# Performance work log

Hardware: AMD Instinct MI355X
Metric: run time of the kernel (lower is better)

## Reference

```python
import math
import jax, jax.numpy as jnp
import numpy as np

CHUNK = 32
PROB_FLOOR = 0.02
EPS = 1e-5

def l2norm(x):
    return x * jax.lax.rsqrt(jnp.sum(x * x, -1, keepdims=True) + 1e-6)

def causal_dwconv(x, w):
    # x: (B, L, C), w: (C, K) depthwise causal FIR (left-padded)
    B, L, C = x.shape
    K = w.shape[-1]
    y = jax.lax.conv_general_dilated(jnp.transpose(x, (0, 2, 1)), w[:, None, :], (1,), [(K - 1, 0)], feature_group_count=C)
    return jnp.transpose(y, (0, 2, 1))

def delta_rule_chunkwise(q, k, v, beta, chunk=CHUNK):
    # q,k: (b,h,L,dk)  v: (b,h,L,dv)  beta: (b,h,L)
    b, h, L, dk = q.shape
    dv = v.shape[-1]
    pad = (-L) % chunk
    if pad:
        q = jnp.pad(q, ((0, 0), (0, 0), (0, pad), (0, 0)))
        k = jnp.pad(k, ((0, 0), (0, 0), (0, pad), (0, 0)))
        v = jnp.pad(v, ((0, 0), (0, 0), (0, pad), (0, 0)))
        beta = jnp.pad(beta, ((0, 0), (0, 0), (0, pad)))
    Lp = L + pad
    n = Lp // chunk
    q = l2norm(q)
    k = l2norm(k)
    v = v * beta[..., None]
    kb = k * beta[..., None]
    r = lambda t: t.reshape(b, h, n, chunk, t.shape[-1])
    q, k, v, kb = (r(q), r(k), r(v), r(kb))
    i_ = jnp.arange(chunk)
    strict_lower = (i_[:, None] > i_[None, :]).astype(q.dtype)
    lower_incl = (i_[:, None] >= i_[None, :]).astype(q.dtype)
    inv = -(kb @ jnp.swapaxes(k, -1, -2)) * strict_lower  # (b,h,n,c,c)
    for i in range(1, chunk):  # row-wise forward substitution; chunk is static so unrolled
        inv = inv.at[..., i, :].add(jnp.einsum('...j,...jk->...k', inv[..., i, :], inv))
    inv = inv + jnp.eye(chunk, dtype=q.dtype)
    u = inv @ v   # (b,h,n,c,dv)
    w = inv @ kb  # (b,h,n,c,dk)
    mv = lambda t: jnp.moveaxis(t, 2, 0)  # scan over chunks
    def step(S, xs):
        qi, ki, ui, wi = xs
        attn = (qi @ jnp.swapaxes(ki, -1, -2)) * lower_incl
        ui2 = ui - wi @ S
        oi = qi @ S + attn @ ui2
        return S + jnp.swapaxes(ki, -1, -2) @ ui2, oi
    S0 = jnp.zeros((b, h, dk, dv), q.dtype)
    S, outs = jax.lax.scan(step, S0, (mv(q), mv(k), mv(u), mv(w)))
    out = jnp.moveaxis(outs, 0, 2).reshape(b, h, Lp, dv)[:, :, :L]
    return out, S

def head_stats(x):
    # x: (B,L,H,D) -> (B,L,4): [mean, var, abs-mean, l2] per head, averaged over heads
    mean = x.mean(-1)
    var = ((x - mean[..., None]) ** 2).mean(-1)
    am = jnp.abs(x).mean(-1)
    l2 = jnp.sqrt((x * x).sum(-1))
    return jnp.stack([mean, var, am, l2], -1).mean(2)

def rmsnorm(x, w):
    return x * jax.lax.rsqrt((x * x).mean(-1, keepdims=True) + EPS) * w

def setup_inputs():
    key = jax.random.key(0)
    ks = jax.random.split(key, 20)
    B, L, D, H = 2, 4096, 1024, 4
    dv = D // H
    f32 = jnp.float32
    rn = lambda k, shape, s: (jax.random.normal(k, shape) * s).astype(f32)
    fir = lambda k, shape: rn(k, shape, 0.02).at[..., -1].add(1.0)  # near-identity causal filter
    return {
        'hidden_states': jax.random.normal(ks[0], (B, L, D), f32),
        'Wq': rn(ks[1], (D, D), 0.02), 'Wk': rn(ks[2], (D, D), 0.02), 'Wv': rn(ks[3], (D, D), 0.02),
        'Wb': rn(ks[4], (D, H), 0.02),
        'wq_conv': fir(ks[5], (D, 4)), 'wk_conv': fir(ks[6], (D, 4)), 'wv_conv': fir(ks[7], (D, 4)),
        'fir_long': fir(ks[8], (H, dv, 64)), 'fir_short': fir(ks[9], (H, dv, 5)),
        'Wg1': rn(ks[10], (D + 16, D), 0.02), 'bg1': jnp.zeros((D,), f32),
        'Wg2': rn(ks[11], (D, 4), 0.02), 'bg2': jnp.array([-0.5, -0.5, 1.0, 3.0], f32),
        'logit_temp': jnp.array([math.log(math.expm1(0.7))], f32),
        'conv_res_logit': jnp.full((H,), -1.0, f32),
        'Wres': rn(ks[12], (D, H), 0.02), 'bres': jnp.full((H,), -1.0, f32),
        'Wog1': rn(ks[13], (D + 8, D // 2), 0.02), 'bog1': jnp.zeros((D // 2,), f32),
        'Wog2': rn(ks[14], (D // 2, 1), 0.02), 'bog2': jnp.full((1,), -1.0986122886681098, f32),
        'norm_w': jnp.ones((dv,), f32),
        'Wo': rn(ks[15], (D, D), 0.02),
    }

def reference(hidden_states, Wq, Wk, Wv, Wb, wq_conv, wk_conv, wv_conv, fir_long, fir_short, Wg1, bg1, Wg2, bg2, logit_temp, conv_res_logit, Wres, bres, Wog1, bog1, Wog2, bog2, norm_w, Wo):
    B, L, D = hidden_states.shape
    H = Wb.shape[-1]
    silu = jax.nn.silu
    q_in = silu(causal_dwconv(hidden_states @ Wq, wq_conv))
    k_in = silu(causal_dwconv(hidden_states @ Wk, wk_conv))
    v_in = silu(causal_dwconv(hidden_states @ Wv, wv_conv))
    dk = q_in.shape[-1] // H
    dv = v_in.shape[-1] // H
    q = q_in.reshape(B, L, H, dk)
    k = k_in.reshape(B, L, H, dk)
    v_direct = v_in.reshape(B, L, H, dv)
    beta = jax.nn.sigmoid(hidden_states @ Wb)  # (B,L,H)
    do, S = delta_rule_chunkwise(jnp.transpose(q, (0, 2, 1, 3)), jnp.transpose(k, (0, 2, 1, 3)), jnp.transpose(v_direct, (0, 2, 1, 3)), jnp.transpose(beta, (0, 2, 1)))
    delta_out = jnp.transpose(do, (0, 2, 1, 3))  # (B,L,H,dv)
    local_long = causal_dwconv(v_in, fir_long.reshape(-1, fir_long.shape[-1])).reshape(B, L, H, dv)
    local_short = causal_dwconv(v_in, fir_short.reshape(-1, fir_short.shape[-1])).reshape(B, L, H, dv)
    stats = jnp.concatenate([head_stats(t) for t in (local_short, local_long, delta_out, v_direct)], -1)  # (B,L,16)
    gate_in = jnp.concatenate([hidden_states, stats], -1)
    logits = (jax.nn.gelu(gate_in @ Wg1 + bg1, approximate=False) @ Wg2 + bg2) / jax.nn.softplus(logit_temp)
    p = jax.nn.softmax(logits, -1)
    p = jnp.clip(p, PROB_FLOOR, None)
    p = p / p.sum(-1, keepdims=True)
    pw = p[:, :, None, :]  # (B,L,1,4)
    o = pw[..., 0:1] * local_short + pw[..., 1:2] * local_long + pw[..., 2:3] * delta_out + pw[..., 3:4] * v_direct
    res_gate = jax.nn.sigmoid(hidden_states @ Wres + bres)  # (B,L,H)
    static = jax.nn.sigmoid(conv_res_logit)  # (H,)
    o = o + (static[None, None, :] * res_gate)[..., None] * local_short
    og_stats = jnp.concatenate([head_stats(o), head_stats(v_direct)], -1)  # (B,L,8)
    og_in = jnp.concatenate([hidden_states, og_stats], -1)
    og = jax.nn.sigmoid(jax.nn.gelu(og_in @ Wog1 + bog1, approximate=False) @ Wog2 + bog2)  # (B,L,1)
    o = o * og[:, :, :, None]
    o = rmsnorm(o, norm_w)
    return o.reshape(B, L, -1) @ Wo
```

## Files before the change

### kernel.cpp

```cpp
#include <hip/hip_runtime.h>
#include <math.h>

#define B_ 2
#define L_ 4096
#define D_ 1024
#define H_ 4
#define DH 256
#define CHUNKSZ 32
#define NCH (L_/CHUNKSZ)
#define BL (B_*L_)
#define BLD (B_*L_*D_)

typedef __attribute__((ext_vector_type(8))) short bf16x8;
typedef __attribute__((ext_vector_type(4))) float f32x4;

__device__ __forceinline__ float sigmf(float x) { return 1.f / (1.f + expf(-x)); }
__device__ __forceinline__ float geluf(float x) { return 0.5f * x * (1.f + erff(x * 0.70710678118654752f)); }
__device__ __forceinline__ unsigned short f2bf(float f) {
  unsigned int u = __float_as_uint(f);
  unsigned int r = (u + 0x7FFFu + ((u >> 16) & 1u)) >> 16;
  return (unsigned short)r;
}
__device__ __forceinline__ unsigned int pk2bf(float a, float b) {
  return ((unsigned int)f2bf(b) << 16) | (unsigned int)f2bf(a);
}

__global__ __launch_bounds__(256)
void wconv_all(const float* __restrict__ Wq, const float* __restrict__ Wk,
               const float* __restrict__ Wv, const float* __restrict__ Wg1,
               const float* __restrict__ Wog1, const float* __restrict__ Wo,
               unsigned short* __restrict__ wtq, unsigned short* __restrict__ wtk,
               unsigned short* __restrict__ wtv, unsigned short* __restrict__ wtg1,
               unsigned short* __restrict__ wtog1, unsigned short* __restrict__ wto) {
  __shared__ float tile[32][33];
  int bid = blockIdx.x;
  const float* W; unsigned short* Wt; int N; int rem;
  if (bid < 5120) {
    int widx = bid >> 10; rem = bid & 1023; N = 1024;
    switch (widx) {
      case 0: W = Wq; Wt = wtq; break;
      case 1: W = Wk; Wt = wtk; break;
      case 2: W = Wv; Wt = wtv; break;
      case 3: W = Wg1; Wt = wtg1; break;
      default: W = Wo; Wt = wto; break;
    }
  } else { rem = bid - 5120; N = 512; W = Wog1; Wt = wtog1; }
  int nT = N >> 5;
  int nb = (rem % nT) * 32, kb = (rem / nT) * 32;
  int tx = threadIdx.x & 31, ty = threadIdx.x >> 5;
  for (int i = 0; i < 32; i += 8)
    tile[ty + i][tx] = W[(long)(kb + ty + i) * N + nb + tx];
  __syncthreads();
  for (int i = 0; i < 32; i += 8)
    Wt[(long)(nb + ty + i) * 1024 + kb + tx] = f2bf(tile[tx][ty + i]);
}

__global__ __launch_bounds__(256)
void cvt_beta(const float* __restrict__ hs, unsigned short* __restrict__ hsb,
              const float* __restrict__ Wb, const float* __restrict__ Wres,
              const float* __restrict__ bres,
              float* __restrict__ beta, float* __restrict__ resg) {
  __shared__ float red[4][8];
  long m = blockIdx.x;
  int tid = threadIdx.x;
  int k0 = tid * 4;
  float4 x = *reinterpret_cast<const float4*>(&hs[m * 1024 + k0]);
  ushort4 o;
  o.x = f2bf(x.x); o.y = f2bf(x.y); o.z = f2bf(x.z); o.w = f2bf(x.w);
  *reinterpret_cast<ushort4*>(&hsb[m * 1024 + k0]) = o;
  float xr[4] = {x.x, x.y, x.z, x.w};
  float ab[4] = {0.f, 0.f, 0.f, 0.f}, ar[4] = {0.f, 0.f, 0.f, 0.f};
#pragma unroll
  for (int j = 0; j < 4; ++j) {
    float4 wb = *reinterpret_cast<const float4*>(&Wb[(long)(k0 + j) * 4]);
    float4 wr = *reinterpret_cast<const float4*>(&Wres[(long)(k0 + j) * 4]);
    ab[0] = fmaf(xr[j], wb.x, ab[0]); ab[1] = fmaf(xr[j], wb.y, ab[1]);
    ab[2] = fmaf(xr[j], wb.z, ab[2]); ab[3] = fmaf(xr[j], wb.w, ab[3]);
    ar[0] = fmaf(xr[j], wr.x, ar[0]); ar[1] = fmaf(xr[j], wr.y, ar[1]);
    ar[2] = fmaf(xr[j], wr.z, ar[2]); ar[3] = fmaf(xr[j], wr.w, ar[3]);
  }
#pragma unroll
  for (int st = 32; st > 0; st >>= 1) {
#pragma unroll
    for (int n = 0; n < 4; ++n) { ab[n] += __shfl_xor(ab[n], st); ar[n] += __shfl_xor(ar[n], st); }
  }
  int w = tid >> 6;
  if ((tid & 63) == 0) {
#pragma unroll
    for (int n = 0; n < 4; ++n) { red[w][n] = ab[n]; red[w][n + 4] = ar[n]; }
  }
  __syncthreads();
  if (tid < 8) {
    float s = red[0][tid] + red[1][tid] + red[2][tid] + red[3][tid];
    if (tid < 4) beta[m * 4 + tid] = sigmf(s);
    else resg[m * 4 + tid - 4] = sigmf(s + bres[tid - 4]);
  }
}

__global__ __launch_bounds__(256)
void gemm_qkv(const unsigned short* __restrict__ A, const unsigned short* __restrict__ Bt,
              float* __restrict__ C0) {
  __shared__ unsigned short Al[128 * 32];
  __shared__ unsigned short Bl[128 * 32];
  const int K = 1024;
  const int nBn = 24;
  int wgid = blockIdx.x;
  int xcd = wgid & 7;
  int local = wgid >> 3;
  int bm = (xcd * 8 + local / nBn) * 128;
  int bn = (local % nBn) * 128;
  float* Cd = C0 + (long)(bn >> 10) * BLD;
  int cbn = bn & 1023;
  int tid = threadIdx.x;
  int lane = tid & 63, wid = tid >> 6;
  int wr = wid >> 1, wc = wid & 1;
  int l15 = lane & 15, l4 = lane >> 4;
  f32x4 acc[4][4];
#pragma unroll
  for (int i = 0; i < 4; ++i)
#pragma unroll
    for (int j = 0; j < 4; ++j) { acc[i][j].x = 0.f; acc[i][j].y = 0.f; acc[i][j].z = 0.f; acc[i][j].w = 0.f; }
  for (int k0 = 0; k0 < K; k0 += 32) {
    __syncthreads();
#pragma unroll
    for (int i = 0; i < 2; ++i) {
      int idx = tid + i * 256;
      int r = idx >> 2, sl = idx & 3;
      int src = sl ^ ((r >> 1) & 3);
      __builtin_amdgcn_global_load_lds(
          (const __attribute__((address_space(1))) unsigned int*)&A[(long)(bm + r) * K + k0 + src * 8],
          (__attribute__((address_space(3))) unsigned int*)&Al[idx * 8], 16, 0, 0);
      __builtin_amdgcn_global_load_lds(
          (const __attribute__((address_space(1))) unsigned int*)&Bt[(long)(bn + r) * K + k0 + src * 8],
          (__attribute__((address_space(3))) unsigned int*)&Bl[idx * 8], 16, 0, 0);
    }
    __syncthreads();
    bf16x8 af[4], bfr[4];
#pragma unroll
    for (int fi = 0; fi < 4; ++fi) {
      int r = wr * 64 + fi * 16 + l15;
      af[fi] = *reinterpret_cast<const bf16x8*>(&Al[r * 32 + (l4 ^ ((r >> 1) & 3)) * 8]);
    }
#pragma unroll
    for (int fj = 0; fj < 4; ++fj) {
      int r = wc * 64 + fj * 16 + l15;
      bfr[fj] = *reinterpret_cast<const bf16x8*>(&Bl[r * 32 + (l4 ^ ((r >> 1) & 3)) * 8]);
    }
#pragma unroll
    for (int fi = 0; fi < 4; ++fi)
#pragma unroll
      for (int fj = 0; fj < 4; ++fj)
        acc[fi][fj] = __builtin_amdgcn_mfma_f32_16x16x32_bf16(af[fi], bfr[fj], acc[fi][fj], 0, 0, 0);
  }
#pragma unroll
  for (int fi = 0; fi < 4; ++fi) {
    int rb = bm + wr * 64 + fi * 16 + l4 * 4;
#pragma unroll
    for (int fj = 0; fj < 4; ++fj) {
      int cb = cbn + wc * 64 + fj * 16 + l15;
#pragma unroll
      for (int j = 0; j < 4; ++j)
        Cd[(long)(rb + j) * 1024 + cb] = acc[fi][fj][j];
    }
  }
}

__global__ __launch_bounds__(256)
void gemm_gateog(const unsigned short* __restrict__ A, const unsigned short* __restrict__ Bt,
                 float* __restrict__ Cg, float* __restrict__ Cog) {
  __shared__ unsigned short Al[128 * 32];
  __shared__ unsigned short Bl[128 * 32];
  const int K = 1024;
  const int nBn = 12;
  int wgid = blockIdx.x;
  int xcd = wgid & 7;
  int local = wgid >> 3;
  int bm = (xcd * 8 + local / nBn) * 128;
  int bn = (local % nBn) * 128;
  float* Cd; int stride, cbn;
  if (bn < 1024) { Cd = Cg; stride = 1024; cbn = bn; }
  else { Cd = Cog; stride = 512; cbn = bn - 1024; }
  int tid = threadIdx.x;
  int lane = tid & 63, wid = tid >> 6;
  int wr = wid >> 1, wc = wid & 1;
  int l15 = lane & 15, l4 = lane >> 4;
  f32x4 acc[4][4];
#pragma unroll
  for (int i = 0; i < 4; ++i)
#pragma unroll
    for (int j = 0; j < 4; ++j) { acc[i][j].x = 0.f; acc[i][j].y = 0.f; acc[i][j].z = 0.f; acc[i][j].w = 0.f; }
  for (int k0 = 0; k0 < K; k0 += 32) {
    __syncthreads();
#pragma unroll
    for (int i = 0; i < 2; ++i) {
      int idx = tid + i * 256;
      int r = idx >> 2, sl = idx & 3;
      int src = sl ^ ((r >> 1) & 3);
      __builtin_amdgcn_global_load_lds(
          (const __attribute__((address_space(1))) unsigned int*)&A[(long)(bm + r) * K + k0 + src * 8],
          (__attribute__((address_space(3))) unsigned int*)&Al[idx * 8], 16, 0, 0);
      __builtin_amdgcn_global_load_lds(
          (const __attribute__((address_space(1))) unsigned int*)&Bt[(long)(bn + r) * K + k0 + src * 8],
          (__attribute__((address_space(3))) unsigned int*)&Bl[idx * 8], 16, 0, 0);
    }
    __syncthreads();
    bf16x8 af[4], bfr[4];
#pragma unroll
    for (int fi = 0; fi < 4; ++fi) {
      int r = wr * 64 + fi * 16 + l15;
      af[fi] = *reinterpret_cast<const bf16x8*>(&Al[r * 32 + (l4 ^ ((r >> 1) & 3)) * 8]);
    }
#pragma unroll
    for (int fj = 0; fj < 4; ++fj) {
      int r = wc * 64 + fj * 16 + l15;
      bfr[fj] = *reinterpret_cast<const bf16x8*>(&Bl[r * 32 + (l4 ^ ((r >> 1) & 3)) * 8]);
    }
#pragma unroll
    for (int fi = 0; fi < 4; ++fi)
#pragma unroll
      for (int fj = 0; fj < 4; ++fj)
        acc[fi][fj] = __builtin_amdgcn_mfma_f32_16x16x32_bf16(af[fi], bfr[fj], acc[fi][fj], 0, 0, 0);
  }
#pragma unroll
  for (int fi = 0; fi < 4; ++fi) {
    int rb = bm + wr * 64 + fi * 16 + l4 * 4;
#pragma unroll
    for (int fj = 0; fj < 4; ++fj) {
      int cb = cbn + wc * 64 + fj * 16 + l15;
#pragma unroll
      for (int j = 0; j < 4; ++j)
        Cd[(long)(rb + j) * stride + cb] = acc[fi][fj][j];
    }
  }
}

__global__ __launch_bounds__(256)
void gemm_bf16(const unsigned short* __restrict__ A, const unsigned short* __restrict__ Bt,
               float* __restrict__ C, int N) {
  __shared__ unsigned short Al[128 * 32];
  __shared__ unsigned short Bl[128 * 32];
  const int K = 1024;
  int nBn = N >> 7;
  int wgid = blockIdx.x;
  int xcd = wgid & 7;
  int local = wgid >> 3;
  int bm = (xcd * 8 + local / nBn) * 128;
  int bn = (local % nBn) * 128;
  int tid = threadIdx.x;
  int lane = tid & 63, wid = tid >> 6;
  int wr = wid >> 1, wc = wid & 1;
  int l15 = lane & 15, l4 = lane >> 4;
  f32x4 acc[4][4];
#pragma unroll
  for (int i = 0; i < 4; ++i)
#pragma unroll
    for (int j = 0; j < 4; ++j) { acc[i][j].x = 0.f; acc[i][j].y = 0.f; acc[i][j].z = 0.f; acc[i][j].w = 0.f; }
  for (int k0 = 0; k0 < K; k0 += 32) {
    __syncthreads();
#pragma unroll
    for (int i = 0; i < 2; ++i) {
      int idx = tid + i * 256;
      int r = idx >> 2, sl = idx & 3;
      int src = sl ^ ((r >> 1) & 3);
      __builtin_amdgcn_global_load_lds(
          (const __attribute__((address_space(1))) unsigned int*)&A[(long)(bm + r) * K + k0 + src * 8],
          (__attribute__((address_space(3))) unsigned int*)&Al[idx * 8], 16, 0, 0);
      __builtin_amdgcn_global_load_lds(
          (const __attribute__((address_space(1))) unsigned int*)&Bt[(long)(bn + r) * K + k0 + src * 8],
          (__attribute__((address_space(3))) unsigned int*)&Bl[idx * 8], 16, 0, 0);
    }
    __syncthreads();
    bf16x8 af[4], bfr[4];
#pragma unroll
    for (int fi = 0; fi < 4; ++fi) {
      int r = wr * 64 + fi * 16 + l15;
      af[fi] = *reinterpret_cast<const bf16x8*>(&Al[r * 32 + (l4 ^ ((r >> 1) & 3)) * 8]);
    }
#pragma unroll
    for (int fj = 0; fj < 4; ++fj) {
      int r = wc * 64 + fj * 16 + l15;
      bfr[fj] = *reinterpret_cast<const bf16x8*>(&Bl[r * 32 + (l4 ^ ((r >> 1) & 3)) * 8]);
    }
#pragma unroll
    for (int fi = 0; fi < 4; ++fi)
#pragma unroll
      for (int fj = 0; fj < 4; ++fj)
        acc[fi][fj] = __builtin_amdgcn_mfma_f32_16x16x32_bf16(af[fi], bfr[fj], acc[fi][fj], 0, 0, 0);
  }
#pragma unroll
  for (int fi = 0; fi < 4; ++fi) {
    int rb = bm + wr * 64 + fi * 16 + l4 * 4;
#pragma unroll
    for (int fj = 0; fj < 4; ++fj) {
      int cb = bn + wc * 64 + fj * 16 + l15;
#pragma unroll
      for (int j = 0; j < 4; ++j)
        C[(long)(rb + j) * N + cb] = acc[fi][fj][j];
    }
  }
}

#define CTL 128
template<int K>
__global__ __launch_bounds__(256)
void dwconv_tiled(const float* __restrict__ x, const float* __restrict__ w,
                  float* __restrict__ y, int do_silu) {
  __shared__ float tile[(CTL + K - 1) * 64];
  int bid = blockIdx.x;
  int ct = bid & 15;
  int lt = (bid >> 4) & 31;
  int b  = bid >> 9;
  int c0 = ct * 64;
  int l0 = lt * CTL;
  int tid = threadIdx.x;
  const int rows = CTL + K - 1;
  for (int i = tid; i < rows * 16; i += 256) {
    int rr = i >> 4, c4 = i & 15;
    int l = l0 - (K - 1) + rr;
    float4 v = make_float4(0.f, 0.f, 0.f, 0.f);
    if (l >= 0) v = *reinterpret_cast<const float4*>(&x[((long)b * L_ + l) * D_ + c0 + c4 * 4]);
    *reinterpret_cast<float4*>(&tile[rr * 64 + c4 * 4]) = v;
  }
  __syncthreads();
  int c = tid & 63;
  int wv = tid >> 6;
  float wreg[K];
#pragma unroll
  for (int j = 0; j < K; ++j) wreg[j] = w[(long)(c0 + c) * K + j];
#pragma unroll
  for (int g = 0; g < 4; ++g) {
    int lo_base = g * 32 + wv * 8;
    float win[8];
#pragma unroll
    for (int r = 0; r < 8; ++r) win[r] = tile[(lo_base + r) * 64 + c];
    float acc[8] = {0.f, 0.f, 0.f, 0.f, 0.f, 0.f, 0.f, 0.f};
#pragma unroll
    for (int j = 0; j < K; ++j) {
#pragma unroll
      for (int r = 0; r < 8; ++r) acc[r] = fmaf(wreg[j], win[r], acc[r]);
      if (j < K - 1) {
#pragma unroll
        for (int r = 0; r < 7; ++r) win[r] = win[r + 1];
        win[7] = tile[(lo_base + j + 8) * 64 + c];
      }
    }
#pragma unroll
    for (int r = 0; r < 8; ++r) {
      float v = acc[r];
      if (do_silu) v = v * sigmf(v);
      y[((long)b * L_ + l0 + lo_base + r) * D_ + c0 + c] = v;
    }
  }
}

__global__ __launch_bounds__(256)
void l2norm_wave2(float* __restrict__ x0, float* __restrict__ x1) {
  int bid = blockIdx.x;
  const int half = BL * H_ / 4;
  float* x = (bid < half) ? x0 : x1;
  int lb = (bid < half) ? bid : bid - half;
  long row = (long)lb * 4 + (threadIdx.x >> 6);
  int lane = threadIdx.x & 63;
  float4 v = *reinterpret_cast<const float4*>(&x[row * 256 + lane * 4]);
  float q = v.x * v.x + v.y * v.y + v.z * v.z + v.w * v.w;
#pragma unroll
  for (int st = 32; st > 0; st >>= 1) q += __shfl_xor(q, st);
  float inv = rsqrtf(q + 1e-6f);
  v.x *= inv; v.y *= inv; v.z *= inv; v.w *= inv;
  *reinterpret_cast<float4*>(&x[row * 256 + lane * 4]) = v;
}

__global__ __launch_bounds__(256)
void chunk_uw(const float* __restrict__ qn, const float* __restrict__ kn,
              const float* __restrict__ v, const float* __restrict__ beta,
              float* __restrict__ u,
              unsigned short* __restrict__ q_bf, unsigned short* __restrict__ w_bf,
              unsigned short* __restrict__ kT_bf, unsigned short* __restrict__ at_bf) {
  __shared__ float skT[256][33];
  __shared__ float sinv[32][33];
  __shared__ float sbeta[32];
  int blk = blockIdx.x;
  int ci = blk % NCH;
  int bh = blk / NCH;
  int h = bh % H_;
  int b = bh / H_;
  long base = ((long)b * L_ + (long)ci * CHUNKSZ) * D_ + h * DH;
  long brow = (long)b * L_ + (long)ci * CHUNKSZ;
  long obase = (long)blk * 8192;
  int tid = threadIdx.x;
  for (int i = tid; i < 32 * 256; i += 256) {
    int r = i >> 8, c = i & 255;
    skT[c][r] = kn[base + (long)r * D_ + c];
  }
  if (tid < 32) sbeta[tid] = beta[(brow + tid) * H_ + h];
  __syncthreads();
  for (int i = tid; i < 8192; i += 256)
    kT_bf[obase + i] = f2bf(skT[i >> 5][i & 31]);
  for (int i = tid; i < 8192; i += 256)
    q_bf[obase + i] = f2bf(qn[base + (long)(i >> 8) * D_ + (i & 255)]);
  int j = tid & 31, i0 = tid >> 5;
  for (int r = 0; r < 4; ++r) {
    int i = i0 + (r << 3);
    float acc = 0.f;
    for (int d = 0; d < 256; ++d) acc += skT[d][i] * skT[d][j];
    sinv[i][j] = (i > j) ? -acc * sbeta[i] : 0.f;
  }
  __syncthreads();
  for (int i = 1; i < 32; ++i) {
    float val = 0.f;
    if (tid < 32) {
      for (int t = 0; t < i; ++t) val += sinv[i][t] * sinv[t][tid];
    }
    __syncthreads();
    if (tid < 32) sinv[i][tid] += val;
    __syncthreads();
  }
  if (tid < 32) sinv[tid][tid] += 1.f;
  long abase = (long)blk * 1024;
  for (int r = 0; r < 4; ++r) {
    int i = i0 + (r << 3);
    const float* qrow = qn + base + (long)i * D_;
    float acc = 0.f;
    for (int d = 0; d < 256; ++d) acc += qrow[d] * skT[d][j];
    at_bf[abase + i * 32 + j] = f2bf((i >= j) ? acc : 0.f);
  }
  __syncthreads();
  int c = tid;
  float vt[32], kt[32];
#pragma unroll
  for (int t = 0; t < 32; ++t) {
    vt[t] = v[base + t * D_ + c] * sbeta[t];
    kt[t] = skT[c][t] * sbeta[t];
  }
#pragma unroll
  for (int i2 = 0; i2 < 32; ++i2) {
    float au = 0.f, aw = 0.f;
#pragma unroll
    for (int t = 0; t <= i2; ++t) {
      float f = sinv[i2][t];
      au += f * vt[t];
      aw += f * kt[t];
    }
    u[base + i2 * D_ + c] = au;
    w_bf[obase + i2 * 256 + c] = f2bf(aw);
  }
}

__global__ __launch_bounds__(64, 1)
void delta_scan(const unsigned short* __restrict__ qb, const unsigned short* __restrict__ wbf,
                const unsigned short* __restrict__ ktb, const unsigned short* __restrict__ atb,
                const float* __restrict__ u, float* __restrict__ out) {
  __shared__ unsigned short sB[16 * 264];
  __shared__ unsigned short su2[16 * 40];
  int blk = blockIdx.x;
  int bh = blk & 7, cg = blk >> 3;
  int h = bh & 3, b = bh >> 2;
  int lane = threadIdx.x;
  int l15 = lane & 15, l4 = lane >> 4;
  int colw = cg * 16;

  f32x4 zero4; zero4.x = 0.f; zero4.y = 0.f; zero4.z = 0.f; zero4.w = 0.f;
  f32x4 acc[16];
#pragma unroll
  for (int t = 0; t < 16; ++t) acc[t] = zero4;

  uint4 wf[2][8];
  float ru[2][4];
  uint4 qf[2][8];
  uint4 kfa[8], kfb[8];
  uint4 af[2];

#define LOAD_W(CI) do {                                                          \
    long o8_ = ((long)bh * NCH + (CI)) * 8192;                                   \
    _Pragma("unroll")                                                            \
    for (int m_ = 0; m_ < 2; ++m_)                                               \
      _Pragma("unroll")                                                          \
      for (int kc_ = 0; kc_ < 8; ++kc_)                                          \
        wf[m_][kc_] = *reinterpret_cast<const uint4*>(                           \
            &wbf[o8_ + (16 * m_ + l15) * 256 + kc_ * 32 + l4 * 8]);              \
  } while (0)

#define LOAD_U(CI) do {                                                          \
    long ub_ = ((long)b * L_ + (long)(CI) * CHUNKSZ) * D_ + h * DH + colw;       \
    _Pragma("unroll")                                                            \
    for (int m_ = 0; m_ < 2; ++m_)                                               \
      _Pragma("unroll")                                                          \
      for (int r_ = 0; r_ < 4; ++r_)                                             \
        ru[m_][r_] = u[ub_ + (long)(16 * m_ + 4 * l4 + r_) * D_ + l15];          \
  } while (0)

#define LOAD_Q(CI) do {                                                          \
    long o8_ = ((long)bh * NCH + (CI)) * 8192;                                   \
    _Pragma("unroll")                                                            \
    for (int m_ = 0; m_ < 2; ++m_)                                               \
      _Pragma("unroll")                                                          \
      for (int kc_ = 0; kc_ < 8; ++kc_)                                          \
        qf[m_][kc_] = *reinterpret_cast<const uint4*>(                           \
            &qb[o8_ + (16 * m_ + l15) * 256 + kc_ * 32 + l4 * 8]);               \
  } while (0)

#define LOAD_KA(CI) do {                                                         \
    long o8_ = ((long)bh * NCH + (CI)) * 8192;                                   \
    _Pragma("unroll")                                                            \
    for (int dt_ = 0; dt_ < 8; ++dt_)                                            \
      kfa[dt_] = *reinterpret_cast<const uint4*>(                                \
          &ktb[o8_ + (16 * dt_ + l15) * 32 + l4 * 8]);                           \
  } while (0)

#define LOAD_KB(CI) do {                                                         \
    long o8_ = ((long)bh * NCH + (CI)) * 8192;                                   \
    _Pragma("unroll")                                                            \
    for (int dt_ = 0; dt_ < 8; ++dt_)                                            \
      kfb[dt_] = *reinterpret_cast<const uint4*>(                                \
          &ktb[o8_ + (16 * (dt_ + 8) + l15) * 32 + l4 * 8]);                     \
  } while (0)

#define LOAD_A(CI) do {                                                          \
    long oa_ = ((long)bh * NCH + (CI)) * 1024;                                   \
    _Pragma("unroll")                                                            \
    for (int m_ = 0; m_ < 2; ++m_)                                               \
      af[m_] = *reinterpret_cast<const uint4*>(                                  \
          &atb[oa_ + (16 * m_ + l15) * 32 + l4 * 8]);                            \
  } while (0)

#define SCAN_BODY(CI, PF) do {                                                   \
    long ub = ((long)b * L_ + (long)(CI) * CHUNKSZ) * D_ + h * DH + colw;        \
    _Pragma("unroll")                                                            \
    for (int dt = 0; dt < 16; ++dt) {                                            \
      uint2 pv;                                                                  \
      pv.x = pk2bf(acc[dt].x, acc[dt].y);                                        \
      pv.y = pk2bf(acc[dt].z, acc[dt].w);                                        \
      *reinterpret_cast<uint2*>(&sB[l15 * 264 + dt * 16 + l4 * 4]) = pv;         \
    }                                                                            \
    bf16x8 sf[8];                                                                \
    _Pragma("unroll")                                                            \
    for (int kc = 0; kc < 8; ++kc)                                               \
      sf[kc] = *reinterpret_cast<const bf16x8*>(&sB[l15 * 264 + kc * 32 + l4 * 8]); \
    f32x4 wa[2][2];                                                              \
    wa[0][0] = zero4; wa[0][1] = zero4; wa[1][0] = zero4; wa[1][1] = zero4;      \
    _Pragma("unroll")                                                            \
    for (int kc = 0; kc < 8; ++kc) {                                             \
      _Pragma("unroll")                                                          \
      for (int m = 0; m < 2; ++m)                                                \
        wa[m][kc & 1] = __builtin_amdgcn_mfma_f32_16x16x32_bf16(                 \
            *reinterpret_cast<bf16x8*>(&wf[m][kc]), sf[kc], wa[m][kc & 1], 0, 0, 0); \
    }                                                                            \
    if (PF) LOAD_W((CI) + 1);                                                    \
    _Pragma("unroll")                                                            \
    for (int m = 0; m < 2; ++m) {                                                \
      f32x4 wsum = wa[m][0] + wa[m][1];                                          \
      uint2 pv;                                                                  \
      pv.x = pk2bf(ru[m][0] - wsum.x, ru[m][1] - wsum.y);                        \
      pv.y = pk2bf(ru[m][2] - wsum.z, ru[m][3] - wsum.w);                        \
      *reinterpret_cast<uint2*>(&su2[l15 * 40 + m * 16 + l4 * 4]) = pv;          \
    }                                                                            \
    if (PF) LOAD_U((CI) + 1);                                                    \
    bf16x8 u2f = *reinterpret_cast<const bf16x8*>(&su2[l15 * 40 + l4 * 8]);      \
    _Pragma("unroll")                                                            \
    for (int dt = 0; dt < 8; ++dt)                                               \
      acc[dt] = __builtin_amdgcn_mfma_f32_16x16x32_bf16(                         \
          *reinterpret_cast<bf16x8*>(&kfa[dt]), u2f, acc[dt], 0, 0, 0);          \
    if (PF) LOAD_KA((CI) + 1);                                                   \
    _Pragma("unroll")                                                            \
    for (int dt = 0; dt < 8; ++dt)                                               \
      acc[dt + 8] = __builtin_amdgcn_mfma_f32_16x16x32_bf16(                     \
          *reinterpret_cast<bf16x8*>(&kfb[dt]), u2f, acc[dt + 8], 0, 0, 0);      \
    if (PF) LOAD_KB((CI) + 1);                                                   \
    f32x4 qa[2][2];                                                              \
    qa[0][0] = zero4; qa[0][1] = zero4; qa[1][0] = zero4; qa[1][1] = zero4;      \
    _Pragma("unroll")                                                            \
    for (int kc = 0; kc < 8; ++kc) {                                             \
      _Pragma("unroll")                                                          \
      for (int m = 0; m < 2; ++m)                                                \
        qa[m][kc & 1] = __builtin_amdgcn_mfma_f32_16x16x32_bf16(                 \
            *reinterpret_cast<bf16x8*>(&qf[m][kc]), sf[kc], qa[m][kc & 1], 0, 0, 0); \
    }                                                                            \
    if (PF) LOAD_Q((CI) + 1);                                                    \
    _Pragma("unroll")                                                            \
    for (int m = 0; m < 2; ++m) {                                                \
      f32x4 qacc = qa[m][0] + qa[m][1];                                          \
      f32x4 dv = __builtin_amdgcn_mfma_f32_16x16x32_bf16(                        \
          *reinterpret_cast<bf16x8*>(&af[m]), u2f, qacc, 0, 0, 0);               \
      _Pragma("unroll")                                                          \
      for (int r = 0; r < 4; ++r)                                                \
        out[ub + (long)(16 * m + 4 * l4 + r) * D_ + l15] = dv[r];                \
    }                                                                            \
    if (PF) LOAD_A((CI) + 1);                                                    \
  } while (0)

  LOAD_W(0); LOAD_U(0); LOAD_Q(0); LOAD_KA(0); LOAD_KB(0); LOAD_A(0);

  for (int ci = 0; ci < NCH - 1; ++ci) {
    SCAN_BODY(ci, 1);
  }
  SCAN_BODY(NCH - 1, 0);

#undef LOAD_W
#undef LOAD_U
#undef LOAD_Q
#undef LOAD_KA
#undef LOAD_KB
#undef LOAD_A
#undef SCAN_BODY
}

__global__ __launch_bounds__(256)
void head_stats4(const float* __restrict__ t0, const float* __restrict__ t1,
                 const float* __restrict__ t2, const float* __restrict__ t3,
                 float* __restrict__ outp) {
  long bl = blockIdx.x;
  int w = threadIdx.x >> 6, lane = threadIdx.x & 63;
  const float* x = (w == 0) ? t0 : (w == 1) ? t1 : (w == 2) ? t2 : t3;
  float m = 0.f, vv = 0.f, am = 0.f, l2 = 0.f;
#pragma unroll
  for (int h = 0; h < 4; ++h) {
    float4 v = *reinterpret_cast<const float4*>(&x[bl * 1024 + h * 256 + lane * 4]);
    float s = v.x + v.y + v.z + v.w;
    float q = v.x * v.x + v.y * v.y + v.z * v.z + v.w * v.w;
    float a = fabsf(v.x) + fabsf(v.y) + fabsf(v.z) + fabsf(v.w);
#pragma unroll
    for (int st = 32; st > 0; st >>= 1) {
      s += __shfl_xor(s, st); q += __shfl_xor(q, st); a += __shfl_xor(a, st);
    }
    float mean = s * (1.f / 256.f);
    m += mean;
    vv += q * (1.f / 256.f) - mean * mean;
    am += a * (1.f / 256.f);
    l2 += sqrtf(q);
  }
  if (lane == 0) {
    float* o = outp + bl * 16 + w * 4;
    o[0] = m * 0.25f; o[1] = vv * 0.25f; o[2] = am * 0.25f; o[3] = l2 * 0.25f;
  }
}

__global__ __launch_bounds__(256)
void gate_fused(const float* __restrict__ g, const float* __restrict__ stats,
                const float* __restrict__ Wg1t, const float* __restrict__ bg1,
                const float* __restrict__ Wg2, const float* __restrict__ bg2,
                const float* __restrict__ temp_in, float* __restrict__ p) {
  __shared__ float red[4][4];
  long m = blockIdx.x;
  int tid = threadIdx.x;
  int c0 = tid * 4;
  float4 gv = *reinterpret_cast<const float4*>(&g[m * 1024 + c0]);
  float st[16];
#pragma unroll
  for (int k = 0; k < 16; ++k) st[k] = stats[m * 16 + k];
  float la[4] = {0.f, 0.f, 0.f, 0.f};
  float gvv[4] = {gv.x, gv.y, gv.z, gv.w};
#pragma unroll
  for (int j = 0; j < 4; ++j) {
    int c = c0 + j;
    float s = gvv[j] + bg1[c];
#pragma unroll
    for (int k = 0; k < 16; ++k) s += st[k] * Wg1t[(long)k * 1024 + c];
    float ge = geluf(s);
#pragma unroll
    for (int n = 0; n < 4; ++n) la[n] += ge * Wg2[c * 4 + n];
  }
#pragma unroll
  for (int stp = 32; stp > 0; stp >>= 1)
#pragma unroll
    for (int n = 0; n < 4; ++n) la[n] += __shfl_xor(la[n], stp);
  int w = tid >> 6;
  if ((tid & 63) == 0) {
#pragma unroll
    for (int n = 0; n < 4; ++n) red[w][n] = la[n];
  }
  __syncthreads();
  if (tid == 0) {
    float temp = log1pf(expf(temp_in[0]));
    float l[4];
#pragma unroll
    for (int n = 0; n < 4; ++n)
      l[n] = (red[0][n] + red[1][n] + red[2][n] + red[3][n] + bg2[n]) / temp;
    float mx = fmaxf(fmaxf(l[0], l[1]), fmaxf(l[2], l[3]));
    float e[4], s = 0.f;
#pragma unroll
    for (int n = 0; n < 4; ++n) { e[n] = expf(l[n] - mx); s += e[n]; }
    float s2 = 0.f;
#pragma unroll
    for (int n = 0; n < 4; ++n) { e[n] = fmaxf(e[n] / s, 0.02f); s2 += e[n]; }
#pragma unroll
    for (int n = 0; n < 4; ++n) p[m * 4 + n] = e[n] / s2;
  }
}

__global__ __launch_bounds__(256)
void combine_ogstats(const float* __restrict__ ls, const float* __restrict__ ll,
                     const float* __restrict__ dd, const float* __restrict__ vd,
                     const float* __restrict__ p, const float* __restrict__ resg,
                     const float* __restrict__ crl, float* __restrict__ o,
                     float* __restrict__ og8) {
  __shared__ float part[4][8];
  long bl = blockIdx.x;
  int h = threadIdx.x >> 6, lane = threadIdx.x & 63;
  long base = bl * 1024 + h * 256 + lane * 4;
  float4 lsv = *reinterpret_cast<const float4*>(&ls[base]);
  float4 llv = *reinterpret_cast<const float4*>(&ll[base]);
  float4 ddv = *reinterpret_cast<const float4*>(&dd[base]);
  float4 vdv = *reinterpret_cast<const float4*>(&vd[base]);
  float p0 = p[bl * 4 + 0], p1 = p[bl * 4 + 1], p2 = p[bl * 4 + 2], p3 = p[bl * 4 + 3];
  float sg = sigmf(crl[h]) * resg[bl * 4 + h];
  float c0 = p0 + sg;
  float4 ov;
  ov.x = c0 * lsv.x + p1 * llv.x + p2 * ddv.x + p3 * vdv.x;
  ov.y = c0 * lsv.y + p1 * llv.y + p2 * ddv.y + p3 * vdv.y;
  ov.z = c0 * lsv.z + p1 * llv.z + p2 * ddv.z + p3 * vdv.z;
  ov.w = c0 * lsv.w + p1 * llv.w + p2 * ddv.w + p3 * vdv.w;
  *reinterpret_cast<float4*>(&o[base]) = ov;
  float s = ov.x + ov.y + ov.z + ov.w;
  float q = ov.x * ov.x + ov.y * ov.y + ov.z * ov.z + ov.w * ov.w;
  float a = fabsf(ov.x) + fabsf(ov.y) + fabsf(ov.z) + fabsf(ov.w);
  float sv = vdv.x + vdv.y + vdv.z + vdv.w;
  float qv = vdv.x * vdv.x + vdv.y * vdv.y + vdv.z * vdv.z + vdv.w * vdv.w;
  float av = fabsf(vdv.x) + fabsf(vdv.y) + fabsf(vdv.z) + fabsf(vdv.w);
#pragma unroll
  for (int st = 32; st > 0; st >>= 1) {
    s += __shfl_xor(s, st); q += __shfl_xor(q, st); a += __shfl_xor(a, st);
    sv += __shfl_xor(sv, st); qv += __shfl_xor(qv, st); av += __shfl_xor(av, st);
  }
  if (lane == 0) {
    float mo = s * (1.f / 256.f), mv = sv * (1.f / 256.f);
    part[h][0] = mo; part[h][1] = q * (1.f / 256.f) - mo * mo;
    part[h][2] = a * (1.f / 256.f); part[h][3] = sqrtf(q);
    part[h][4] = mv; part[h][5] = qv * (1.f / 256.f) - mv * mv;
    part[h][6] = av * (1.f / 256.f); part[h][7] = sqrtf(qv);
  }
  __syncthreads();
  if (threadIdx.x < 8) {
    int t = threadIdx.x;
    og8[bl * 8 + t] = 0.25f * (part[0][t] + part[1][t] + part[2][t] + part[3][t]);
  }
}

__global__ __launch_bounds__(256)
void og_gate_fused(const float* __restrict__ g, const float* __restrict__ og8,
                   const float* __restrict__ Wog1t, const float* __restrict__ bog1,
                   const float* __restrict__ Wog2, const float* __restrict__ bog2,
                   float* __restrict__ ogv) {
  __shared__ float red[4];
  long m = blockIdx.x;
  int tid = threadIdx.x;
  int c0 = tid * 2;
  float2 gv = *reinterpret_cast<const float2*>(&g[m * 512 + c0]);
  float st[8];
#pragma unroll
  for (int k = 0; k < 8; ++k) st[k] = og8[m * 8 + k];
  float a = 0.f;
  float gvv[2] = {gv.x, gv.y};
#pragma unroll
  for (int j = 0; j < 2; ++j) {
    int c = c0 + j;
    float s = gvv[j] + bog1[c];
#pragma unroll
    for (int k = 0; k < 8; ++k) s += st[k] * Wog1t[(long)k * 512 + c];
    a += geluf(s) * Wog2[c];
  }
#pragma unroll
  for (int stp = 32; stp > 0; stp >>= 1) a += __shfl_xor(a, stp);
  int w = tid >> 6;
  if ((tid & 63) == 0) red[w] = a;
  __syncthreads();
  if (tid == 0) ogv[m] = sigmf(red[0] + red[1] + red[2] + red[3] + bog2[0]);
}

__global__ __launch_bounds__(256)
void scale_rmsnorm_bf16(const float* __restrict__ o, const float* __restrict__ og,
                        const float* __restrict__ nw, unsigned short* __restrict__ xb) {
  long row = (long)blockIdx.x * 4 + (threadIdx.x >> 6);
  long bl = row >> 2;
  int lane = threadIdx.x & 63;
  float g = og[bl];
  float4 v = *reinterpret_cast<const float4*>(&o[row * 256 + lane * 4]);
  v.x *= g; v.y *= g; v.z *= g; v.w *= g;
  float q = v.x * v.x + v.y * v.y + v.z * v.z + v.w * v.w;
#pragma unroll
  for (int st = 32; st > 0; st >>= 1) q += __shfl_xor(q, st);
  float scale = rsqrtf(q * (1.f / 256.f) + 1e-5f);
  float4 w4 = *reinterpret_cast<const float4*>(&nw[lane * 4]);
  ushort4 r;
  r.x = f2bf(v.x * scale * w4.x);
  r.y = f2bf(v.y * scale * w4.y);
  r.z = f2bf(v.z * scale * w4.z);
  r.w = f2bf(v.w * scale * w4.w);
  *reinterpret_cast<ushort4*>(&xb[row * 256 + lane * 4]) = r;
}

extern "C" void kernel_launch(void* const* d_in, const int* in_sizes, int n_in,
                              void* d_out, int out_size, void* d_ws, size_t ws_size,
                              hipStream_t stream) {
  const float* hs       = (const float*)d_in[0];
  const float* Wq       = (const float*)d_in[1];
  const float* Wk       = (const float*)d_in[2];
  const float* Wv       = (const float*)d_in[3];
  const float* Wb       = (const float*)d_in[4];
  const float* wq_conv  = (const float*)d_in[5];
  const float* wk_conv  = (const float*)d_in[6];
  const float* wv_conv  = (const float*)d_in[7];
  const float* fir_long = (const float*)d_in[8];
  const float* fir_short= (const float*)d_in[9];
  const float* Wg1      = (const float*)d_in[10];
  const float* bg1      = (const float*)d_in[11];
  const float* Wg2      = (const float*)d_in[12];
  const float* bg2      = (const float*)d_in[13];
  const float* logit_temp     = (const float*)d_in[14];
  const float* conv_res_logit = (const float*)d_in[15];
  const float* Wres     = (const float*)d_in[16];
  const float* bres     = (const float*)d_in[17];
  const float* Wog1     = (const float*)d_in[18];
  const float* bog1     = (const float*)d_in[19];
  const float* Wog2     = (const float*)d_in[20];
  const float* bog2     = (const float*)d_in[21];
  const float* norm_w   = (const float*)d_in[22];
  const float* Wo       = (const float*)d_in[23];
  float* out = (float*)d_out;
  float* ws = (float*)d_ws;

  float* b0 = ws;
  float* b1 = ws + 1L * BLD;
  float* b2 = ws + 2L * BLD;
  float* b3 = ws + 3L * BLD;
  float* b4 = ws + 4L * BLD;
  float* sm = ws + 5L * BLD;
  float* beta    = sm;
  float* resg    = beta + BL * H_;
  float* stats16 = resg + BL * H_;
  float* og8     = stats16 + BL * 16;
  float* logits  = og8 + BL * 8;
  float* pbuf    = logits + BL * 4;
  float* ogv     = pbuf + BL * 4;
  unsigned short* q_bfg  = (unsigned short*)(ogv + BL);
  unsigned short* kT_bfg = q_bfg + (long)BLD;
  unsigned short* at_bfg = kT_bfg + (long)BLD;
  unsigned short* hsb  = at_bfg + 1024L * 1024;
  unsigned short* wtq  = hsb + (long)BLD;
  unsigned short* wtk  = wtq + 1024L * 1024;
  unsigned short* wtv  = wtk + 1024L * 1024;
  unsigned short* wtg1 = wtv + 1024L * 1024;
  unsigned short* wtog1= wtg1 + 1024L * 1024;
  unsigned short* wto  = wtog1 + 512L * 1024;
  unsigned short* w_bfg = (unsigned short*)b4;
  unsigned short* xb    = q_bfg;
  float* ogh = (float*)q_bfg;

  size_t needed = (5L * BLD + BL * 41) * 4
                + (3L * BLD + 1024L * 1024 + 5L * 1024 * 1024 + 512L * 1024) * 2;
  if (ws_size < needed) return;

  dim3 blk(256);
  wconv_all<<<5632, blk, 0, stream>>>(Wq, Wk, Wv, Wg1, Wog1, Wo, wtq, wtk, wtv, wtg1, wtog1, wto);
  cvt_beta<<<BL, blk, 0, stream>>>(hs, hsb, Wb, Wres, bres, beta, resg);
  gemm_qkv<<<1536, blk, 0, stream>>>(hsb, wtq, b0);
  dwconv_tiled<4><<<1024, blk, 0, stream>>>(b0, wq_conv, b3, 1);
  dwconv_tiled<4><<<1024, blk, 0, stream>>>(b1, wk_conv, b0, 1);
  dwconv_tiled<4><<<1024, blk, 0, stream>>>(b2, wv_conv, b1, 1);
  l2norm_wave2<<<2 * BL * H_ / 4, blk, 0, stream>>>(b3, b0);
  chunk_uw<<<B_ * H_ * NCH, blk, 0, stream>>>(b3, b0, b1, beta, b2, q_bfg, w_bfg, kT_bfg, at_bfg);
  delta_scan<<<128, dim3(64), 0, stream>>>(q_bfg, w_bfg, kT_bfg, at_bfg, b2, b2);
  dwconv_tiled<64><<<1024, blk, 0, stream>>>(b1, fir_long, b3, 0);
  dwconv_tiled<5><<<1024, blk, 0, stream>>>(b1, fir_short, b4, 0);
  head_stats4<<<BL, blk, 0, stream>>>(b4, b3, b2, b1, stats16);
  gemm_gateog<<<768, blk, 0, stream>>>(hsb, wtg1, b0, ogh);
  gate_fused<<<BL, blk, 0, stream>>>(b0, stats16, Wg1 + 1024L * 1024, bg1, Wg2, bg2, logit_temp, pbuf);
  combine_ogstats<<<BL, blk, 0, stream>>>(b4, b3, b2, b1, pbuf, resg, conv_res_logit, b0, og8);
  og_gate_fused<<<BL, blk, 0, stream>>>(ogh, og8, Wog1 + 1024L * 512, bog1, Wog2, bog2, ogv);
  scale_rmsnorm_bf16<<<BL * H_ / 4, blk, 0, stream>>>(b0, ogv, norm_w, xb);
  gemm_bf16<<<512, blk, 0, stream>>>(xb, wto, out, 1024);
}
```

Measured before the change: 806.6 us.

## Fuse qkv convs, fold l2norm into chunk_uw, merge FIR convs

The three short causal convolutions for q, k and v now run in one launch, as do the long and short FIR convolutions. The separate l2norm pass is removed: chunk_uw computes per-row inverse norms for q and k and applies them as scale factors on the outputs and dot products. Buffers are reassigned, and the output tensor is reused as scratch for the conv'd v. This saves launches and a full read/write pass over q and k, at the cost of extra work in chunk_uw and reduced occupancy in the FIR kernel, which allocates shared memory sized for the long 64-tap filter in every block.

Result: faster. 777.4 us (-3.6%).

```diff
diff --git a/kernel.cpp b/kernel.cpp
--- a/kernel.cpp
+++ b/kernel.cpp
@@ -302,14 +302,11 @@
 
 #define CTL 128
 template<int K>
-__global__ __launch_bounds__(256)
-void dwconv_tiled(const float* __restrict__ x, const float* __restrict__ w,
-                  float* __restrict__ y, int do_silu) {
-  __shared__ float tile[(CTL + K - 1) * 64];
-  int bid = blockIdx.x;
-  int ct = bid & 15;
-  int lt = (bid >> 4) & 31;
-  int b  = bid >> 9;
+__device__ __forceinline__ void dwconv_body(const float* __restrict__ x, const float* __restrict__ w,
+                                            float* __restrict__ y, int rem, float* tile, int do_silu) {
+  int ct = rem & 15;
+  int lt = (rem >> 4) & 31;
+  int b  = rem >> 9;
   int c0 = ct * 64;
   int l0 = lt * CTL;
   int tid = threadIdx.x;
@@ -354,20 +351,27 @@
 }
 
 __global__ __launch_bounds__(256)
-void l2norm_wave2(float* __restrict__ x0, float* __restrict__ x1) {
+void dwconv_qkv(const float* __restrict__ xq, const float* __restrict__ xk,
+                const float* __restrict__ xv,
+                const float* __restrict__ wq, const float* __restrict__ wk,
+                const float* __restrict__ wv,
+                float* __restrict__ yq, float* __restrict__ yk, float* __restrict__ yv) {
+  __shared__ float tile[(CTL + 3) * 64];
   int bid = blockIdx.x;
-  const int half = BL * H_ / 4;
-  float* x = (bid < half) ? x0 : x1;
-  int lb = (bid < half) ? bid : bid - half;
-  long row = (long)lb * 4 + (threadIdx.x >> 6);
-  int lane = threadIdx.x & 63;
-  float4 v = *reinterpret_cast<const float4*>(&x[row * 256 + lane * 4]);
-  float q = v.x * v.x + v.y * v.y + v.z * v.z + v.w * v.w;
-#pragma unroll
-  for (int st = 32; st > 0; st >>= 1) q += __shfl_xor(q, st);
-  float inv = rsqrtf(q + 1e-6f);
-  v.x *= inv; v.y *= inv; v.z *= inv; v.w *= inv;
-  *reinterpret_cast<float4*>(&x[row * 256 + lane * 4]) = v;
+  int sel = bid >> 10, rem = bid & 1023;
+  const float* x = (sel == 0) ? xq : (sel == 1) ? xk : xv;
+  const float* w = (sel == 0) ? wq : (sel == 1) ? wk : wv;
+  float* y = (sel == 0) ? yq : (sel == 1) ? yk : yv;
+  dwconv_body<4>(x, w, y, rem, tile, 1);
+}
+
+__global__ __launch_bounds__(256)
+void dwconv_fir(const float* __restrict__ v, const float* __restrict__ wl,
+                const float* __restrict__ ws5, float* __restrict__ yl, float* __restrict__ ys) {
+  __shared__ float tile[(CTL + 63) * 64];
+  int bid = blockIdx.x;
+  if (bid < 1024) dwconv_body<64>(v, wl, yl, bid, tile, 0);
+  else dwconv_body<5>(v, ws5, ys, bid - 1024, tile, 0);
 }
 
 __global__ __launch_bounds__(256)
@@ -379,6 +383,7 @@
   __shared__ float skT[256][33];
   __shared__ float sinv[32][33];
   __shared__ float sbeta[32];
+  __shared__ float knorm[32], qnorm[32];
   int blk = blockIdx.x;
   int ci = blk % NCH;
   int bh = blk / NCH;
@@ -394,16 +399,31 @@
   }
   if (tid < 32) sbeta[tid] = beta[(brow + tid) * H_ + h];
   __syncthreads();
+  {
+    int row = tid >> 3, seg = tid & 7;
+    float s = 0.f;
+    for (int c2 = seg * 32; c2 < seg * 32 + 32; ++c2) { float xv = skT[c2][row]; s = fmaf(xv, xv, s); }
+    s += __shfl_xor(s, 1); s += __shfl_xor(s, 2); s += __shfl_xor(s, 4);
+    if (seg == 0) knorm[row] = rsqrtf(s + 1e-6f);
+    const float* qr = qn + base + (long)row * D_;
+    float sq = 0.f;
+    for (int c2 = seg * 32; c2 < seg * 32 + 32; ++c2) { float xv = qr[c2]; sq = fmaf(xv, xv, sq); }
+    sq += __shfl_xor(sq, 1); sq += __shfl_xor(sq, 2); sq += __shfl_xor(sq, 4);
+    if (seg == 0) qnorm[row] = rsqrtf(sq + 1e-6f);
+  }
+  __syncthreads();
   for (int i = tid; i < 8192; i += 256)
-    kT_bf[obase + i] = f2bf(skT[i >> 5][i & 31]);
-  for (int i = tid; i < 8192; i += 256)
-    q_bf[obase + i] = f2bf(qn[base + (long)(i >> 8) * D_ + (i & 255)]);
+    kT_bf[obase + i] = f2bf(skT[i >> 5][i & 31] * knorm[i & 31]);
+  for (int i = tid; i < 8192; i += 256) {
+    int r = i >> 8, c = i & 255;
+    q_bf[obase + i] = f2bf(qn[base + (long)r * D_ + c] * qnorm[r]);
+  }
   int j = tid & 31, i0 = tid >> 5;
   for (int r = 0; r < 4; ++r) {
     int i = i0 + (r << 3);
     float acc = 0.f;
     for (int d = 0; d < 256; ++d) acc += skT[d][i] * skT[d][j];
-    sinv[i][j] = (i > j) ? -acc * sbeta[i] : 0.f;
+    sinv[i][j] = (i > j) ? -acc * knorm[i] * knorm[j] * sbeta[i] : 0.f;
   }
   __syncthreads();
   for (int i = 1; i < 32; ++i) {
@@ -422,7 +442,7 @@
     const float* qrow = qn + base + (long)i * D_;
     float acc = 0.f;
     for (int d = 0; d < 256; ++d) acc += qrow[d] * skT[d][j];
-    at_bf[abase + i * 32 + j] = f2bf((i >= j) ? acc : 0.f);
+    at_bf[abase + i * 32 + j] = f2bf((i >= j) ? acc * qnorm[i] * knorm[j] : 0.f);
   }
   __syncthreads();
   int c = tid;
@@ -430,7 +450,7 @@
 #pragma unroll
   for (int t = 0; t < 32; ++t) {
     vt[t] = v[base + t * D_ + c] * sbeta[t];
-    kt[t] = skT[c][t] * sbeta[t];
+    kt[t] = skT[c][t] * knorm[t] * sbeta[t];
   }
 #pragma unroll
   for (int i2 = 0; i2 < 32; ++i2) {
@@ -841,9 +861,10 @@
   unsigned short* wtg1 = wtv + 1024L * 1024;
   unsigned short* wtog1= wtg1 + 1024L * 1024;
   unsigned short* wto  = wtog1 + 512L * 1024;
-  unsigned short* w_bfg = (unsigned short*)b4;
+  unsigned short* w_bfg = (unsigned short*)b0;
   unsigned short* xb    = q_bfg;
   float* ogh = (float*)q_bfg;
+  float* vsc = out;
 
   size_t needed = (5L * BLD + BL * 41) * 4
                 + (3L * BLD + 1024L * 1024 + 5L * 1024 * 1024 + 512L * 1024) * 2;
@@ -853,18 +874,14 @@
   wconv_all<<<5632, blk, 0, stream>>>(Wq, Wk, Wv, Wg1, Wog1, Wo, wtq, wtk, wtv, wtg1, wtog1, wto);
   cvt_beta<<<BL, blk, 0, stream>>>(hs, hsb, Wb, Wres, bres, beta, resg);
   gemm_qkv<<<1536, blk, 0, stream>>>(hsb, wtq, b0);
-  dwconv_tiled<4><<<1024, blk, 0, stream>>>(b0, wq_conv, b3, 1);
-  dwconv_tiled<4><<<1024, blk, 0, stream>>>(b1, wk_conv, b0, 1);
-  dwconv_tiled<4><<<1024, blk, 0, stream>>>(b2, wv_conv, b1, 1);
-  l2norm_wave2<<<2 * BL * H_ / 4, blk, 0, stream>>>(b3, b0);
-  chunk_uw<<<B_ * H_ * NCH, blk, 0, stream>>>(b3, b0, b1, beta, b2, q_bfg, w_bfg, kT_bfg, at_bfg);
+  dwconv_qkv<<<3072, blk, 0, stream>>>(b0, b1, b2, wq_conv, wk_conv, wv_conv, b3, b4, vsc);
+  chunk_uw<<<B_ * H_ * NCH, blk, 0, stream>>>(b3, b4, vsc, beta, b2, q_bfg, w_bfg, kT_bfg, at_bfg);
   delta_scan<<<128, dim3(64), 0, stream>>>(q_bfg, w_bfg, kT_bfg, at_bfg, b2, b2);
-  dwconv_tiled<64><<<1024, blk, 0, stream>>>(b1, fir_long, b3, 0);
-  dwconv_tiled<5><<<1024, blk, 0, stream>>>(b1, fir_short, b4, 0);
-  head_stats4<<<BL, blk, 0, stream>>>(b4, b3, b2, b1, stats16);
-  gemm_gateog<<<768, blk, 0, stream>>>(hsb, wtg1, b0, ogh);
-  gate_fused<<<BL, blk, 0, stream>>>(b0, stats16, Wg1 + 1024L * 1024, bg1, Wg2, bg2, logit_temp, pbuf);
-  combine_ogstats<<<BL, blk, 0, stream>>>(b4, b3, b2, b1, pbuf, resg, conv_res_logit, b0, og8);
+  dwconv_fir<<<2048, blk, 0, stream>>>(vsc, fir_long, fir_short, b3, b1);
+  head_stats4<<<BL, blk, 0, stream>>>(b1, b3, b2, vsc, stats16);
+  gemm_gateog<<<768, blk, 0, stream>>>(hsb, wtg1, b4, ogh);
+  gate_fused<<<BL, blk, 0, stream>>>(b4, stats16, Wg1 + 1024L * 1024, bg1, Wg2, bg2, logit_temp, pbuf);
+  combine_ogstats<<<BL, blk, 0, stream>>>(b1, b3, b2, vsc, pbuf, resg, conv_res_logit, b0, og8);
   og_gate_fused<<<BL, blk, 0, stream>>>(ogh, og8, Wog1 + 1024L * 512, bog1, Wog2, bog2, ogv);
   scale_rmsnorm_bf16<<<BL * H_ / 4, blk, 0, stream>>>(b0, ogv, norm_w, xb);
   gemm_bf16<<<512, blk, 0, stream>>>(xb, wto, out, 1024);
```
